# Optimization experiments

Hardware: AMD Instinct MI355X
Metric: run time of the kernel (lower is better)

The kernel has to match this reference:

```python
import jax, jax.numpy as jnp
import numpy as np

# --- Config (Kimi/DeepSeek-style fine-grained MoE) ---
T = 4096        # num tokens
H = 1024        # hidden_size
I = 512         # moe_intermediate_size
E = 64          # num_experts
K = 8           # num_experts_per_token (top_k)
NG = 8          # num_expert_group
TKG = 4         # topk_group
NSH = 2         # num_shared_experts
IS = I * NSH    # shared-expert intermediate size
ROUTED_SCALE = 2.5


def setup_inputs() -> dict:
    key = jax.random.key(0)
    ks = jax.random.split(key, 7)
    s = 0.02
    return {
        "hidden_states": jax.random.normal(ks[0], (T, H), jnp.float32),
        "gate_w": jax.random.normal(ks[1], (E, H), jnp.float32) * s,          # router
        "e_bias": jax.random.normal(ks[2], (E,), jnp.float32) * 0.01,          # e_score_correction_bias
        "w1": jax.random.normal(ks[3], (E, H, 2 * I), jnp.float32) * s,       # per-expert gate_up
        "w2": jax.random.normal(ks[4], (E, I, H), jnp.float32) * s,           # per-expert down
        "sw_gu": jax.random.normal(ks[5], (H, 2 * IS), jnp.float32) * s,      # shared gate_up
        "sw_d": jax.random.normal(ks[6], (IS, H), jnp.float32) * s,           # shared down
    }


def _silu_and_mul(gu):
    d = gu.shape[-1] // 2
    return jax.nn.silu(gu[..., :d]) * gu[..., d:]


def _grouped_topk(scores, e_bias):
    """DeepSeek-V3/Kimi grouped top-k with sigmoid scoring + score-correction bias."""
    Tn = scores.shape[0]
    sfc = scores + e_bias[None, :]                       # scores_for_choice [T, E]
    # group score = sum of top-2 corrected scores inside each group
    grp = sfc.reshape(Tn, NG, E // NG)
    group_scores = jax.lax.top_k(grp, 2)[0].sum(-1)      # [T, NG]
    gidx = jax.lax.top_k(group_scores, TKG)[1]           # [T, TKG]
    gmask = jnp.zeros((Tn, NG), sfc.dtype).at[jnp.arange(Tn)[:, None], gidx].set(1.0)
    smask = jnp.repeat(gmask, E // NG, axis=1) > 0       # [T, E] bool
    tmp = jnp.where(smask, sfc, 0.0)                     # masked_fill(~mask, 0.0) as in vLLM
    topk_ids = jax.lax.top_k(tmp, K)[1]                  # [T, K]
    topk_w = jnp.take_along_axis(scores, topk_ids, axis=1)
    topk_w = topk_w / topk_w.sum(-1, keepdims=True)      # renormalize
    return topk_w, topk_ids


def _forward(x, gate_w, e_bias, w1, w2, sw_gu, sw_d):
    Tn, Hn = x.shape
    # shared experts (KimiMLP)
    shared = _silu_and_mul(x @ sw_gu) @ sw_d             # [T, H]
    # router
    logits = x @ gate_w.T                                # [T, E]
    scores = jax.nn.sigmoid(logits)
    topk_w, topk_ids = _grouped_topk(scores, e_bias)
    # dispatch: sort the T*K assignments by expert id -> grouped GEMM
    flat_ids = topk_ids.reshape(-1)                      # [T*K]
    order = jnp.argsort(flat_ids)                        # [T*K]
    tok = order // K                                     # token index of each sorted assignment
    xs = x[tok]                                          # [T*K, H] gathered tokens
    gsizes = jnp.bincount(flat_ids, length=E).astype(jnp.int32)
    gu = jax.lax.ragged_dot(xs, w1, gsizes)              # [T*K, 2I] grouped GEMM
    h = _silu_and_mul(gu)                                # [T*K, I]
    ys = jax.lax.ragged_dot(h, w2, gsizes)               # [T*K, H]
    # combine: scale by routing weight, scatter-add back to tokens
    flat_w = topk_w.reshape(-1)[order]                   # [T*K]
    routed = jnp.zeros((Tn, Hn), x.dtype).at[tok].add(ys * flat_w[:, None])
    return routed * ROUTED_SCALE + shared


def reference(hidden_states, gate_w, e_bias, w1, w2, sw_gu, sw_d):
    return _forward(hidden_states, gate_w, e_bias, w1, w2, sw_gu, sw_d)
```

## Files before the change

kernel.cpp:

```cpp
#include <hip/hip_runtime.h>
#include <cstdint>
#include <cstddef>

#define TT   4096
#define HH   1024
#define II   512
#define EE   64
#define KT   8
#define ISZ  1024
#define TKA  32768
#define TKAP (TKA + 2048)
#define MAXT 320

typedef __bf16 bf16x8 __attribute__((ext_vector_type(8)));
typedef float  f32x4  __attribute__((ext_vector_type(4)));
typedef unsigned short us8v __attribute__((ext_vector_type(8)));

__device__ __forceinline__ unsigned short f2bf(float f) {
  unsigned u = __float_as_uint(f);
  u += 0x7fffu + ((u >> 16) & 1u);
  return (unsigned short)(u >> 16);
}

#define GLDS(gp, lp) __builtin_amdgcn_global_load_lds( \
    (const __attribute__((address_space(1))) void*)(gp), \
    (__attribute__((address_space(3))) void*)(lp), 16, 0, 0)


__global__ __launch_bounds__(256) void k_transpose(const float* __restrict__ in,
                                                   unsigned short* __restrict__ out,
                                                   int R, int C) {
  __shared__ float tile[64][65];
  long b = blockIdx.z;
  int r0 = blockIdx.x * 64, c0 = blockIdx.y * 64;
  const float* ip = in + b * (long)R * C;
  unsigned short* op = out + b * (long)R * C;
  int tc = threadIdx.x & 63, tr = threadIdx.x >> 6;
#pragma unroll
  for (int rr = 0; rr < 64; rr += 4)
    tile[tr + rr][tc] = ip[(long)(r0 + tr + rr) * C + (c0 + tc)];
  __syncthreads();
  int kt = R >> 5;
#pragma unroll
  for (int p = 0; p < 2; p++) {
    int sid = p * 256 + threadIdx.x;
    int nl = sid >> 3, kq = sid & 7;
    int n = c0 + nl;
    int kg = r0 + kq * 8;
    int s = ((kq & 3) + ((n >> 1) & 3)) & 3;
    long off = ((long)(n >> 4) * kt + (kg >> 5)) * 512 + (n & 15) * 32 + s * 8;
    us8v v;
#pragma unroll
    for (int j = 0; j < 8; j++) v[j] = f2bf(tile[kq * 8 + j][nl]);
    *(us8v*)(op + off) = v;
  }
}

__global__ __launch_bounds__(256) void k_cvt(const float* __restrict__ in,
                                             unsigned short* __restrict__ out) {
  int i = blockIdx.x * 256 + threadIdx.x;
  float4 v = ((const float4*)in)[i];
  ushort4 o;
  o.x = f2bf(v.x); o.y = f2bf(v.y); o.z = f2bf(v.z); o.w = f2bf(v.w);
  ((ushort4*)out)[i] = o;
}

__global__ __launch_bounds__(256) void k_router(const float* __restrict__ x,
    const float* __restrict__ gw, const float* __restrict__ eb,
    int* __restrict__ topk_ids, float* __restrict__ topk_w, int* __restrict__ counts)
{
  __shared__ float xrow[HH];
  __shared__ float sc[EE];
  int t = blockIdx.x;
  int tid = threadIdx.x;
  for (int i = tid; i < HH; i += 256) xrow[i] = x[(long)t * HH + i];
  __syncthreads();
  int e = tid >> 2, q = tid & 3;
  const float* w = gw + (long)e * HH;
  double acc = 0.0, acc2 = 0.0;
  for (int i = q * 8; i < HH; i += 32) {
    float4 wa = *(const float4*)(w + i);
    float4 wb = *(const float4*)(w + i + 4);
    acc  += (double)wa.x * (double)xrow[i]
          + (double)wa.y * (double)xrow[i + 1]
          + (double)wa.z * (double)xrow[i + 2]
          + (double)wa.w * (double)xrow[i + 3];
    acc2 += (double)wb.x * (double)xrow[i + 4]
          + (double)wb.y * (double)xrow[i + 5]
          + (double)wb.z * (double)xrow[i + 6]
          + (double)wb.w * (double)xrow[i + 7];
  }
  acc += acc2;
  acc += __shfl_down(acc, 2);
  acc += __shfl_down(acc, 1);
  if (q == 0) sc[e] = (float)(1.0 / (1.0 + exp(-acc)));
  __syncthreads();
  if (tid < 64) {
    int lane = tid;
    float s = sc[lane];
    float sfc = s + eb[lane];
    float m1 = sfc, m2 = -1e30f;
#pragma unroll
    for (int d = 1; d < 8; d <<= 1) {
      float o1 = __shfl_xor(m1, d);
      float o2 = __shfl_xor(m2, d);
      float hi = fmaxf(m1, o1);
      float lo = fminf(m1, o1);
      m2 = fmaxf(lo, fmaxf(m2, o2));
      m1 = hi;
    }
    float gs = m1 + m2;
    int g = lane >> 3;
    int grank = 0;
#pragma unroll
    for (int j = 0; j < 8; j++) {
      float gj = __shfl(gs, j * 8);
      if (gj > gs || (gj == gs && j < g)) grank++;
    }
    bool gsel = grank < 4;
    float mv = gsel ? sfc : 0.0f;
    int rank = 0;
    for (int j = 0; j < 64; j++) {
      float vj = __shfl(mv, j);
      if (vj > mv || (vj == mv && j < lane)) rank++;
    }
    bool sel = rank < KT;
    float ssum = sel ? s : 0.0f;
#pragma unroll
    for (int d = 1; d < 64; d <<= 1) ssum += __shfl_xor(ssum, d);
    unsigned long long bal = __ballot(sel);
    if (sel) {
      int pos = __popcll(bal & ((1ull << lane) - 1ull));
      topk_ids[(long)t * KT + pos] = lane;
      topk_w[(long)t * KT + pos] = s / ssum;
      atomicAdd(&counts[lane], 1);
    }
  }
}

__global__ void k_offsets(const int* __restrict__ counts, int* __restrict__ offsets,
                          int* __restrict__ cursor, int* __restrict__ tile_e,
                          int* __restrict__ tile_r0, int* __restrict__ perm,
                          float* __restrict__ wslot)
{
  int lane = threadIdx.x;
  int c = counts[lane];
  int ca = (c + 15) & ~15;
  int xs = ca;
#pragma unroll
  for (int d = 1; d < 64; d <<= 1) { int y = __shfl_up(xs, d); if (lane >= d) xs += y; }
  int off = xs - ca;
  offsets[lane] = off;
  cursor[lane] = off;
  if (lane == 63) offsets[EE] = xs;
  int nt = (c + 127) >> 7;
  int tp = nt;
#pragma unroll
  for (int d = 1; d < 64; d <<= 1) { int y = __shfl_up(tp, d); if (lane >= d) tp += y; }
  int tbase = tp - nt;
  for (int i = 0; i < nt; i++) { tile_e[tbase + i] = lane; tile_r0[tbase + i] = off + i * 128; }
  int total = __shfl(tp, 63);
  for (int i = total + lane; i < MAXT; i += 64) tile_e[i] = -1;
  for (int i = off + c; i < off + ca; i++) { perm[i] = 0; wslot[i] = 0.f; }
  int ptotal = __shfl(xs, 63);
  int lastEnd = __shfl(off + nt * 128, 63);
  for (int i = ptotal + lane; i < lastEnd; i += 64) { perm[i] = 0; wslot[i] = 0.f; }
}

__global__ __launch_bounds__(256) void k_scatter(const int* __restrict__ ids,
    const float* __restrict__ tw, int* __restrict__ cursor,
    int* __restrict__ perm, float* __restrict__ wslot, int* __restrict__ inv)
{
  int a = blockIdx.x * 256 + threadIdx.x;
  int e = ids[a];
  int pos = atomicAdd(&cursor[e], 1);
  perm[pos] = a >> 3;
  wslot[pos] = tw[a];
  inv[a] = pos;
}

__global__ __launch_bounds__(256) void k_gemm_gu(
    const unsigned short* __restrict__ Abase, const int* __restrict__ perm,
    const unsigned short* __restrict__ Bbase, long eStride, int Kd, int upOff,
    unsigned short* __restrict__ Hout,
    const int* __restrict__ tile_e, const int* __restrict__ tile_r0,
    const int* __restrict__ eoff, int rowsTotal)
{
  __shared__ __align__(16) unsigned short lds[24576];
  int D = blockIdx.y * gridDim.x + blockIdx.x;
  int cx = D & 7, jj = D >> 3;
  int chunk = gridDim.x >> 3;
  int mt = cx * chunk + jj / gridDim.y;
  int ny = jj - (jj / gridDim.y) * gridDim.y;
  int e = 0, row0, end;
  if (tile_e) {
    e = tile_e[mt];
    if (e < 0) return;
    row0 = tile_r0[mt];
    end = eoff[e + 1];
  } else { row0 = mt * 128; end = rowsTotal; }
  const unsigned short* B = Bbase + (long)e * eStride;
  int n0 = ny * 64;
  int tid = threadIdx.x, lane = tid & 63, wave = tid >> 6;
  int wm = wave >> 1, wn = wave & 1;
  int lr = lane >> 2;
  int lkq = ((((lane & 3) - ((lane >> 3) & 3)) & 3)) * 8;
  int r0a = row0 + wave * 32 + lr;
  int r1a = r0a + 16;
  int t0 = r0a < rowsTotal ? r0a : rowsTotal - 1;
  int t1 = r1a < rowsTotal ? r1a : rowsTotal - 1;
  if (perm) { t0 = perm[t0]; t1 = perm[t1]; }
  const unsigned short* ap0 = Abase + (long)t0 * Kd + lkq;
  const unsigned short* ap1 = Abase + (long)t1 * Kd + lkq;
  int nkt = Kd >> 5;
  const unsigned short* bgp = Bbase + (long)e * eStride
      + ((long)((n0 >> 4) + wave) * nkt) * 512 + lane * 8;
  const unsigned short* bup = Bbase + (long)e * eStride
      + ((long)(((upOff + n0) >> 4) + wave) * nkt) * 512 + lane * 8;
  (void)B;
  unsigned short* lA0 = lds + wave * 1024 + lane * 8;
  unsigned short* lBg = lds + 4096 + wave * 512 + lane * 8;
  unsigned short* lBu = lds + 6144 + wave * 512 + lane * 8;
  f32x4 acc[4][4];
  f32x4 z = {0.f, 0.f, 0.f, 0.f};
  for (int i = 0; i < 4; i++) for (int j = 0; j < 4; j++) acc[i][j] = z;
  int quad = lane >> 4, cl = lane & 15;
  int sw8 = ((quad + ((cl >> 1) & 3)) & 3) * 8;
  int nk = Kd >> 5;
  GLDS(ap0, lA0);             GLDS(ap1, lA0 + 512);
  GLDS(bgp, lBg);             GLDS(bup, lBu);
  GLDS(ap0 + 32, lA0 + 8192); GLDS(ap1 + 32, lA0 + 8192 + 512);
  GLDS(bgp + 512, lBg + 8192); GLDS(bup + 512, lBu + 8192);
  int cur = 0, nxt = 8192, fut = 16384;
  for (int t = 0; t < nk; ++t) {
    __builtin_amdgcn_s_barrier();
    if (t + 2 < nk) {
      int k2 = (t + 2) << 5;
      GLDS(ap0 + k2, lA0 + fut); GLDS(ap1 + k2, lA0 + fut + 512);
      GLDS(bgp + (long)(t + 2) * 512, lBg + fut);
      GLDS(bup + (long)(t + 2) * 512, lBu + fut);
      asm volatile("s_waitcnt vmcnt(8)" ::: "memory");
    } else if (t + 1 < nk) {
      asm volatile("s_waitcnt vmcnt(4)" ::: "memory");
    } else {
      asm volatile("s_waitcnt vmcnt(0)" ::: "memory");
    }
    __builtin_amdgcn_s_barrier();
    asm volatile("" ::: "memory");
    bf16x8 af[4], bgf[2], buf2[2];
#pragma unroll
    for (int mi = 0; mi < 4; mi++)
      af[mi] = *(const bf16x8*)(lds + cur + (wm * 64 + mi * 16 + cl) * 32 + sw8);
#pragma unroll
    for (int ni = 0; ni < 2; ni++) {
      bgf[ni]  = *(const bf16x8*)(lds + cur + 4096 + (wn * 32 + ni * 16 + cl) * 32 + sw8);
      buf2[ni] = *(const bf16x8*)(lds + cur + 6144 + (wn * 32 + ni * 16 + cl) * 32 + sw8);
    }
#pragma unroll
    for (int mi = 0; mi < 4; mi++) {
#pragma unroll
      for (int ni = 0; ni < 2; ni++) {
        acc[mi][ni]     = __builtin_amdgcn_mfma_f32_16x16x32_bf16(af[mi], bgf[ni],  acc[mi][ni],     0, 0, 0);
        acc[mi][ni + 2] = __builtin_amdgcn_mfma_f32_16x16x32_bf16(af[mi], buf2[ni], acc[mi][ni + 2], 0, 0, 0);
      }
    }
    asm volatile("" ::: "memory");
    int tmp = cur; cur = nxt; nxt = fut; fut = tmp;
  }
  int ntO = upOff >> 5;
#pragma unroll
  for (int mi = 0; mi < 4; mi++) {
#pragma unroll
    for (int j = 0; j < 2; j++) {
#pragma unroll
      for (int r = 0; r < 4; r++) {
        int row = row0 + wm * 64 + mi * 16 + quad * 4 + r;
        if (row < end) {
          float g = acc[mi][j][r], u = acc[mi][j + 2][r];
          float hv = g * (1.f / (1.f + __expf(-g))) * u;
          int col = n0 + wn * 32 + j * 16 + cl;
          int sl = (((col >> 3) & 3) + ((row >> 1) & 3)) & 3;
          long offp = ((long)(row >> 4) * ntO + (col >> 5)) * 512
                    + (row & 15) * 32 + sl * 8 + (col & 7);
          Hout[offp] = f2bf(hv);
        }
      }
    }
  }
}

__global__ __launch_bounds__(256) void k_gemm_down(
    const unsigned short* __restrict__ Abase,
    const unsigned short* __restrict__ Bbase, long eStride, int Kd,
    void* __restrict__ Outv, const float* __restrict__ wslot,
    const int* __restrict__ tile_e, const int* __restrict__ tile_r0,
    const int* __restrict__ eoff, int rowsTotal, int mode)
{
  __shared__ __align__(16) unsigned short lds[24576];
  int D = blockIdx.y * gridDim.x + blockIdx.x;
  int cx = D & 7, jj = D >> 3;
  int chunk = gridDim.x >> 3;
  int mt = cx * chunk + jj / gridDim.y;
  int ny = jj - (jj / gridDim.y) * gridDim.y;
  int e = 0, row0, end;
  if (tile_e) {
    e = tile_e[mt];
    if (e < 0) return;
    row0 = tile_r0[mt];
    end = eoff[e + 1];
  } else { row0 = mt * 128; end = rowsTotal; }
  int n0 = ny * 128;
  int tid = threadIdx.x, lane = tid & 63, wave = tid >> 6;
  int wm = wave >> 1, wn = wave & 1;
  int nkt = Kd >> 5;
  long sstep = (long)nkt * 512;
  const unsigned short* apk = Abase
      + ((long)((row0 >> 4) + 2 * wave) * nkt) * 512 + lane * 8;
  const unsigned short* bpk = Bbase + (long)e * eStride
      + ((long)((n0 >> 4) + 2 * wave) * nkt) * 512 + lane * 8;
  unsigned short* lA0 = lds + wave * 1024 + lane * 8;
  unsigned short* lB0 = lds + 4096 + wave * 1024 + lane * 8;
  f32x4 acc[4][4];
  f32x4 z = {0.f, 0.f, 0.f, 0.f};
  for (int i = 0; i < 4; i++) for (int j = 0; j < 4; j++) acc[i][j] = z;
  int quad = lane >> 4, cl = lane & 15;
  int sw8 = ((quad + ((cl >> 1) & 3)) & 3) * 8;
  int nk = Kd >> 5;
  GLDS(apk, lA0);              GLDS(apk + sstep, lA0 + 512);
  GLDS(bpk, lB0);              GLDS(bpk + sstep, lB0 + 512);
  GLDS(apk + 512, lA0 + 8192); GLDS(apk + sstep + 512, lA0 + 8192 + 512);
  GLDS(bpk + 512, lB0 + 8192); GLDS(bpk + sstep + 512, lB0 + 8192 + 512);
  int cur = 0, nxt = 8192, fut = 16384;
  for (int t = 0; t < nk; ++t) {
    __builtin_amdgcn_s_barrier();
    if (t + 2 < nk) {
      long k2 = (long)(t + 2) * 512;
      GLDS(apk + k2, lA0 + fut); GLDS(apk + sstep + k2, lA0 + fut + 512);
      GLDS(bpk + k2, lB0 + fut); GLDS(bpk + sstep + k2, lB0 + fut + 512);
      asm volatile("s_waitcnt vmcnt(8)" ::: "memory");
    } else if (t + 1 < nk) {
      asm volatile("s_waitcnt vmcnt(4)" ::: "memory");
    } else {
      asm volatile("s_waitcnt vmcnt(0)" ::: "memory");
    }
    __builtin_amdgcn_s_barrier();
    asm volatile("" ::: "memory");
    bf16x8 af[4], bfr[4];
#pragma unroll
    for (int mi = 0; mi < 4; mi++)
      af[mi] = *(const bf16x8*)(lds + cur + (wm * 64 + mi * 16 + cl) * 32 + sw8);
#pragma unroll
    for (int ni = 0; ni < 4; ni++)
      bfr[ni] = *(const bf16x8*)(lds + cur + 4096 + (wn * 64 + ni * 16 + cl) * 32 + sw8);
#pragma unroll
    for (int mi = 0; mi < 4; mi++)
#pragma unroll
      for (int ni = 0; ni < 4; ni++)
        acc[mi][ni] = __builtin_amdgcn_mfma_f32_16x16x32_bf16(af[mi], bfr[ni], acc[mi][ni], 0, 0, 0);
    asm volatile("" ::: "memory");
    int tmp = cur; cur = nxt; nxt = fut; fut = tmp;
  }
#pragma unroll
  for (int mi = 0; mi < 4; mi++) {
    int rowb = row0 + wm * 64 + mi * 16 + quad * 4;
#pragma unroll
    for (int r = 0; r < 4; r++) {
      int row = rowb + r;
      if (row >= end) continue;
      if (mode) {
        unsigned short* Y = (unsigned short*)Outv;
        float scale = wslot[row] * 2.5f;
#pragma unroll
        for (int ni = 0; ni < 4; ni++) {
          int col = n0 + wn * 64 + ni * 16 + cl;
          Y[(long)row * HH + col] = f2bf(acc[mi][ni][r] * scale);
        }
      } else {
        float* O = (float*)Outv;
#pragma unroll
        for (int ni = 0; ni < 4; ni++) {
          int col = n0 + wn * 64 + ni * 16 + cl;
          O[(long)row * HH + col] = acc[mi][ni][r];
        }
      }
    }
  }
}

__global__ __launch_bounds__(256) void k_combine(const unsigned short* __restrict__ ys,
    const int* __restrict__ inv, float* __restrict__ out)
{
  int idx = blockIdx.x * 256 + threadIdx.x;
  int t = idx >> 7, c0 = (idx & 127) << 3;
  const int* ip = inv + (long)t * KT;
  float* op = out + (long)t * HH + c0;
  float4 o0 = *(float4*)op;
  float4 o1 = *(float4*)(op + 4);
  float a[8] = {o0.x, o0.y, o0.z, o0.w, o1.x, o1.y, o1.z, o1.w};
#pragma unroll
  for (int k = 0; k < KT; k++) {
    us8v v = *(const us8v*)(ys + (long)ip[k] * HH + c0);
#pragma unroll
    for (int j = 0; j < 8; j++) a[j] += __uint_as_float((unsigned)v[j] << 16);
  }
  *(float4*)op = make_float4(a[0], a[1], a[2], a[3]);
  *(float4*)(op + 4) = make_float4(a[4], a[5], a[6], a[7]);
}

extern "C" void kernel_launch(void* const* d_in, const int* in_sizes, int n_in,
                              void* d_out, int out_size, void* d_ws, size_t ws_size,
                              hipStream_t stream)
{
  const float* x   = (const float*)d_in[0];
  const float* gw  = (const float*)d_in[1];
  const float* eb  = (const float*)d_in[2];
  const float* w1  = (const float*)d_in[3];
  const float* w2  = (const float*)d_in[4];
  const float* sgu = (const float*)d_in[5];
  const float* sd  = (const float*)d_in[6];
  float* out = (float*)d_out;
  char* ws = (char*)d_ws;
  size_t off = 0;
  auto alloc = [&](size_t b) { void* p = ws + off; off += (b + 255) & ~(size_t)255; return p; };
  unsigned short* w1t  = (unsigned short*)alloc((size_t)EE * 2 * II * HH * 2);
  unsigned short* w2t  = (unsigned short*)alloc((size_t)EE * HH * II * 2);
  unsigned short* sgut = (unsigned short*)alloc((size_t)2 * ISZ * HH * 2);
  unsigned short* sdt  = (unsigned short*)alloc((size_t)HH * ISZ * 2);
  unsigned short* xb   = (unsigned short*)alloc((size_t)TT * HH * 2);
  unsigned short* hsb  = (unsigned short*)alloc((size_t)TT * ISZ * 2);
  unsigned short* hb   = (unsigned short*)alloc((size_t)TKAP * II * 2);
  unsigned short* ys   = (unsigned short*)alloc((size_t)TKAP * HH * 2);
  int*   tids   = (int*)alloc((size_t)TKA * 4);
  float* tw     = (float*)alloc((size_t)TKA * 4);
  int*   counts = (int*)alloc(256);
  int*   offs   = (int*)alloc(512);
  int*   cursor = (int*)alloc(256);
  int*   tile_e = (int*)alloc(MAXT * 4);
  int*   tile_r = (int*)alloc(MAXT * 4);
  int*   perm   = (int*)alloc((size_t)TKAP * 4);
  float* wslot  = (float*)alloc((size_t)TKAP * 4);
  int*   inv    = (int*)alloc((size_t)TKA * 4);

  hipMemsetAsync(counts, 0, 256, stream);
  dim3 b256(256);
  k_transpose<<<dim3(HH / 64, (2 * II) / 64, EE), b256, 0, stream>>>(w1, w1t, HH, 2 * II);
  k_transpose<<<dim3(II / 64, HH / 64, EE), b256, 0, stream>>>(w2, w2t, II, HH);
  k_transpose<<<dim3(HH / 64, (2 * ISZ) / 64, 1), b256, 0, stream>>>(sgu, sgut, HH, 2 * ISZ);
  k_transpose<<<dim3(ISZ / 64, HH / 64, 1), b256, 0, stream>>>(sd, sdt, ISZ, HH);
  k_cvt<<<dim3((TT * HH) / 1024), b256, 0, stream>>>(x, xb);
  k_router<<<dim3(TT), b256, 0, stream>>>(x, gw, eb, tids, tw, counts);
  k_offsets<<<dim3(1), dim3(64), 0, stream>>>(counts, offs, cursor, tile_e, tile_r, perm, wslot);
  k_scatter<<<dim3(TKA / 256), b256, 0, stream>>>(tids, tw, cursor, perm, wslot, inv);
  k_gemm_gu<<<dim3(MAXT, II / 64), b256, 0, stream>>>(xb, perm, w1t, (long)2 * II * HH, HH, II,
                                                      hb, tile_e, tile_r, offs, TKAP);
  k_gemm_down<<<dim3(MAXT, HH / 128), b256, 0, stream>>>(hb, w2t, (long)HH * II, II, (void*)ys,
                                                         wslot, tile_e, tile_r, offs, TKAP, 1);
  k_gemm_gu<<<dim3(TT / 128, ISZ / 64), b256, 0, stream>>>(xb, nullptr, sgut, 0, HH, ISZ,
                                                           hsb, nullptr, nullptr, nullptr, TT);
  k_gemm_down<<<dim3(TT / 128, HH / 128), b256, 0, stream>>>(hsb, sdt, 0, ISZ, (void*)out,
                                                             nullptr, nullptr, nullptr, nullptr, TT, 0);
  k_combine<<<dim3(TT * 128 / 256), b256, 0, stream>>>(ys, inv, out);
}
```

Before: 859.4 us.

## Load B weight fragments directly to registers, halve LDS and raise occupancy

Both grouped GEMM kernels stop staging the expert weight (B) tiles through LDS. Each wave now loads its pre-swizzled B fragments straight from global memory into registers, prefetching one k-step ahead. Only the A tile stays triple-buffered in LDS, which halves shared memory, and launch bounds ask for 4 blocks per CU. The B fragments are no longer shared between the two waves that use them, so redundant global/L2 traffic and register pressure rise, and the vmcnt wait counts are retuned to match the new number of loads in flight.

```diff
diff --git a/kernel.cpp b/kernel.cpp
--- a/kernel.cpp
+++ b/kernel.cpp
@@ -179,14 +179,14 @@
   inv[a] = pos;
 }
 
-__global__ __launch_bounds__(256) void k_gemm_gu(
+__global__ __launch_bounds__(256, 4) void k_gemm_gu(
     const unsigned short* __restrict__ Abase, const int* __restrict__ perm,
     const unsigned short* __restrict__ Bbase, long eStride, int Kd, int upOff,
     unsigned short* __restrict__ Hout,
     const int* __restrict__ tile_e, const int* __restrict__ tile_r0,
     const int* __restrict__ eoff, int rowsTotal)
 {
-  __shared__ __align__(16) unsigned short lds[24576];
+  __shared__ __align__(16) unsigned short lds[12288];
   int D = blockIdx.y * gridDim.x + blockIdx.x;
   int cx = D & 7, jj = D >> 3;
   int chunk = gridDim.x >> 3;
@@ -199,7 +199,6 @@
     row0 = tile_r0[mt];
     end = eoff[e + 1];
   } else { row0 = mt * 128; end = rowsTotal; }
-  const unsigned short* B = Bbase + (long)e * eStride;
   int n0 = ny * 64;
   int tid = threadIdx.x, lane = tid & 63, wave = tid >> 6;
   int wm = wave >> 1, wn = wave & 1;
@@ -213,58 +212,61 @@
   const unsigned short* ap0 = Abase + (long)t0 * Kd + lkq;
   const unsigned short* ap1 = Abase + (long)t1 * Kd + lkq;
   int nkt = Kd >> 5;
-  const unsigned short* bgp = Bbase + (long)e * eStride
-      + ((long)((n0 >> 4) + wave) * nkt) * 512 + lane * 8;
-  const unsigned short* bup = Bbase + (long)e * eStride
-      + ((long)(((upOff + n0) >> 4) + wave) * nkt) * 512 + lane * 8;
-  (void)B;
+  int quad = lane >> 4, cl = lane & 15;
+  int sw8 = ((quad + ((cl >> 1) & 3)) & 3) * 8;
+  long fragoff = (long)cl * 32 + sw8;
+  long ebase = (long)e * eStride;
+  const unsigned short* Bg0 = Bbase + ebase + ((long)((n0 >> 4) + wn * 2)     * nkt) * 512 + fragoff;
+  const unsigned short* Bg1 = Bbase + ebase + ((long)((n0 >> 4) + wn * 2 + 1) * nkt) * 512 + fragoff;
+  const unsigned short* Bu0 = Bbase + ebase + ((long)(((upOff + n0) >> 4) + wn * 2)     * nkt) * 512 + fragoff;
+  const unsigned short* Bu1 = Bbase + ebase + ((long)(((upOff + n0) >> 4) + wn * 2 + 1) * nkt) * 512 + fragoff;
   unsigned short* lA0 = lds + wave * 1024 + lane * 8;
-  unsigned short* lBg = lds + 4096 + wave * 512 + lane * 8;
-  unsigned short* lBu = lds + 6144 + wave * 512 + lane * 8;
   f32x4 acc[4][4];
   f32x4 z = {0.f, 0.f, 0.f, 0.f};
   for (int i = 0; i < 4; i++) for (int j = 0; j < 4; j++) acc[i][j] = z;
-  int quad = lane >> 4, cl = lane & 15;
-  int sw8 = ((quad + ((cl >> 1) & 3)) & 3) * 8;
   int nk = Kd >> 5;
   GLDS(ap0, lA0);             GLDS(ap1, lA0 + 512);
-  GLDS(bgp, lBg);             GLDS(bup, lBu);
-  GLDS(ap0 + 32, lA0 + 8192); GLDS(ap1 + 32, lA0 + 8192 + 512);
-  GLDS(bgp + 512, lBg + 8192); GLDS(bup + 512, lBu + 8192);
-  int cur = 0, nxt = 8192, fut = 16384;
+  GLDS(ap0 + 32, lA0 + 4096); GLDS(ap1 + 32, lA0 + 4096 + 512);
+  asm volatile("" ::: "memory");
+  bf16x8 cg0 = *(const bf16x8*)(Bg0);
+  bf16x8 cg1 = *(const bf16x8*)(Bg1);
+  bf16x8 cu0 = *(const bf16x8*)(Bu0);
+  bf16x8 cu1 = *(const bf16x8*)(Bu1);
+  int cur = 0, nxt = 4096, fut = 8192;
   for (int t = 0; t < nk; ++t) {
     __builtin_amdgcn_s_barrier();
     if (t + 2 < nk) {
       int k2 = (t + 2) << 5;
       GLDS(ap0 + k2, lA0 + fut); GLDS(ap1 + k2, lA0 + fut + 512);
-      GLDS(bgp + (long)(t + 2) * 512, lBg + fut);
-      GLDS(bup + (long)(t + 2) * 512, lBu + fut);
       asm volatile("s_waitcnt vmcnt(8)" ::: "memory");
     } else if (t + 1 < nk) {
+      asm volatile("s_waitcnt vmcnt(6)" ::: "memory");
+    } else {
       asm volatile("s_waitcnt vmcnt(4)" ::: "memory");
-    } else {
-      asm volatile("s_waitcnt vmcnt(0)" ::: "memory");
     }
     __builtin_amdgcn_s_barrier();
     asm volatile("" ::: "memory");
-    bf16x8 af[4], bgf[2], buf2[2];
+    bf16x8 ng0, ng1, nu0, nu1;
+    if (t + 1 < nk) {
+      long o = (long)(t + 1) * 512;
+      ng0 = *(const bf16x8*)(Bg0 + o);
+      ng1 = *(const bf16x8*)(Bg1 + o);
+      nu0 = *(const bf16x8*)(Bu0 + o);
+      nu1 = *(const bf16x8*)(Bu1 + o);
+    }
+    bf16x8 af[4];
 #pragma unroll
     for (int mi = 0; mi < 4; mi++)
       af[mi] = *(const bf16x8*)(lds + cur + (wm * 64 + mi * 16 + cl) * 32 + sw8);
 #pragma unroll
-    for (int ni = 0; ni < 2; ni++) {
-      bgf[ni]  = *(const bf16x8*)(lds + cur + 4096 + (wn * 32 + ni * 16 + cl) * 32 + sw8);
-      buf2[ni] = *(const bf16x8*)(lds + cur + 6144 + (wn * 32 + ni * 16 + cl) * 32 + sw8);
-    }
-#pragma unroll
     for (int mi = 0; mi < 4; mi++) {
-#pragma unroll
-      for (int ni = 0; ni < 2; ni++) {
-        acc[mi][ni]     = __builtin_amdgcn_mfma_f32_16x16x32_bf16(af[mi], bgf[ni],  acc[mi][ni],     0, 0, 0);
-        acc[mi][ni + 2] = __builtin_amdgcn_mfma_f32_16x16x32_bf16(af[mi], buf2[ni], acc[mi][ni + 2], 0, 0, 0);
-      }
+      acc[mi][0] = __builtin_amdgcn_mfma_f32_16x16x32_bf16(af[mi], cg0, acc[mi][0], 0, 0, 0);
+      acc[mi][1] = __builtin_amdgcn_mfma_f32_16x16x32_bf16(af[mi], cg1, acc[mi][1], 0, 0, 0);
+      acc[mi][2] = __builtin_amdgcn_mfma_f32_16x16x32_bf16(af[mi], cu0, acc[mi][2], 0, 0, 0);
+      acc[mi][3] = __builtin_amdgcn_mfma_f32_16x16x32_bf16(af[mi], cu1, acc[mi][3], 0, 0, 0);
     }
     asm volatile("" ::: "memory");
+    if (t + 1 < nk) { cg0 = ng0; cg1 = ng1; cu0 = nu0; cu1 = nu1; }
     int tmp = cur; cur = nxt; nxt = fut; fut = tmp;
   }
   int ntO = upOff >> 5;
@@ -289,14 +291,14 @@
   }
 }
 
-__global__ __launch_bounds__(256) void k_gemm_down(
+__global__ __launch_bounds__(256, 4) void k_gemm_down(
     const unsigned short* __restrict__ Abase,
     const unsigned short* __restrict__ Bbase, long eStride, int Kd,
     void* __restrict__ Outv, const float* __restrict__ wslot,
     const int* __restrict__ tile_e, const int* __restrict__ tile_r0,
     const int* __restrict__ eoff, int rowsTotal, int mode)
 {
-  __shared__ __align__(16) unsigned short lds[24576];
+  __shared__ __align__(16) unsigned short lds[12288];
   int D = blockIdx.y * gridDim.x + blockIdx.x;
   int cx = D & 7, jj = D >> 3;
   int chunk = gridDim.x >> 3;
@@ -316,48 +318,61 @@
   long sstep = (long)nkt * 512;
   const unsigned short* apk = Abase
       + ((long)((row0 >> 4) + 2 * wave) * nkt) * 512 + lane * 8;
-  const unsigned short* bpk = Bbase + (long)e * eStride
-      + ((long)((n0 >> 4) + 2 * wave) * nkt) * 512 + lane * 8;
+  int quad = lane >> 4, cl = lane & 15;
+  int sw8 = ((quad + ((cl >> 1) & 3)) & 3) * 8;
+  long fragoff = (long)cl * 32 + sw8;
+  long ebase = (long)e * eStride;
+  const unsigned short* Bf0 = Bbase + ebase + ((long)((n0 >> 4) + wn * 4)     * nkt) * 512 + fragoff;
+  const unsigned short* Bf1 = Bbase + ebase + ((long)((n0 >> 4) + wn * 4 + 1) * nkt) * 512 + fragoff;
+  const unsigned short* Bf2 = Bbase + ebase + ((long)((n0 >> 4) + wn * 4 + 2) * nkt) * 512 + fragoff;
+  const unsigned short* Bf3 = Bbase + ebase + ((long)((n0 >> 4) + wn * 4 + 3) * nkt) * 512 + fragoff;
   unsigned short* lA0 = lds + wave * 1024 + lane * 8;
-  unsigned short* lB0 = lds + 4096 + wave * 1024 + lane * 8;
   f32x4 acc[4][4];
   f32x4 z = {0.f, 0.f, 0.f, 0.f};
   for (int i = 0; i < 4; i++) for (int j = 0; j < 4; j++) acc[i][j] = z;
-  int quad = lane >> 4, cl = lane & 15;
-  int sw8 = ((quad + ((cl >> 1) & 3)) & 3) * 8;
   int nk = Kd >> 5;
   GLDS(apk, lA0);              GLDS(apk + sstep, lA0 + 512);
-  GLDS(bpk, lB0);              GLDS(bpk + sstep, lB0 + 512);
-  GLDS(apk + 512, lA0 + 8192); GLDS(apk + sstep + 512, lA0 + 8192 + 512);
-  GLDS(bpk + 512, lB0 + 8192); GLDS(bpk + sstep + 512, lB0 + 8192 + 512);
-  int cur = 0, nxt = 8192, fut = 16384;
+  GLDS(apk + 512, lA0 + 4096); GLDS(apk + sstep + 512, lA0 + 4096 + 512);
+  asm volatile("" ::: "memory");
+  bf16x8 cb0 = *(const bf16x8*)(Bf0);
+  bf16x8 cb1 = *(const bf16x8*)(Bf1);
+  bf16x8 cb2 = *(const bf16x8*)(Bf2);
+  bf16x8 cb3 = *(const bf16x8*)(Bf3);
+  int cur = 0, nxt = 4096, fut = 8192;
   for (int t = 0; t < nk; ++t) {
     __builtin_amdgcn_s_barrier();
     if (t + 2 < nk) {
       long k2 = (long)(t + 2) * 512;
       GLDS(apk + k2, lA0 + fut); GLDS(apk + sstep + k2, lA0 + fut + 512);
-      GLDS(bpk + k2, lB0 + fut); GLDS(bpk + sstep + k2, lB0 + fut + 512);
       asm volatile("s_waitcnt vmcnt(8)" ::: "memory");
     } else if (t + 1 < nk) {
+      asm volatile("s_waitcnt vmcnt(6)" ::: "memory");
+    } else {
       asm volatile("s_waitcnt vmcnt(4)" ::: "memory");
-    } else {
-      asm volatile("s_waitcnt vmcnt(0)" ::: "memory");
     }
     __builtin_amdgcn_s_barrier();
     asm volatile("" ::: "memory");
-    bf16x8 af[4], bfr[4];
+    bf16x8 nb0, nb1, nb2, nb3;
+    if (t + 1 < nk) {
+      long o = (long)(t + 1) * 512;
+      nb0 = *(const bf16x8*)(Bf0 + o);
+      nb1 = *(const bf16x8*)(Bf1 + o);
+      nb2 = *(const bf16x8*)(Bf2 + o);
+      nb3 = *(const bf16x8*)(Bf3 + o);
+    }
+    bf16x8 af[4];
 #pragma unroll
     for (int mi = 0; mi < 4; mi++)
       af[mi] = *(const bf16x8*)(lds + cur + (wm * 64 + mi * 16 + cl) * 32 + sw8);
 #pragma unroll
-    for (int ni = 0; ni < 4; ni++)
-      bfr[ni] = *(const bf16x8*)(lds + cur + 4096 + (wn * 64 + ni * 16 + cl) * 32 + sw8);
-#pragma unroll
-    for (int mi = 0; mi < 4; mi++)
-#pragma unroll
-      for (int ni = 0; ni < 4; ni++)
-        acc[mi][ni] = __builtin_amdgcn_mfma_f32_16x16x32_bf16(af[mi], bfr[ni], acc[mi][ni], 0, 0, 0);
+    for (int mi = 0; mi < 4; mi++) {
+      acc[mi][0] = __builtin_amdgcn_mfma_f32_16x16x32_bf16(af[mi], cb0, acc[mi][0], 0, 0, 0);
+      acc[mi][1] = __builtin_amdgcn_mfma_f32_16x16x32_bf16(af[mi], cb1, acc[mi][1], 0, 0, 0);
+      acc[mi][2] = __builtin_amdgcn_mfma_f32_16x16x32_bf16(af[mi], cb2, acc[mi][2], 0, 0, 0);
+      acc[mi][3] = __builtin_amdgcn_mfma_f32_16x16x32_bf16(af[mi], cb3, acc[mi][3], 0, 0, 0);
+    }
     asm volatile("" ::: "memory");
+    if (t + 1 < nk) { cb0 = nb0; cb1 = nb1; cb2 = nb2; cb3 = nb3; }
     int tmp = cur; cur = nxt; nxt = fut; fut = tmp;
   }
 #pragma unroll
```

Result: slower. 898.6 us (+4.6%).
